# Performance work log

Measured on AMD Instinct MI355X. Metric: run time of the kernel, lower is better.

## Reference

```python
import jax, jax.numpy as jnp
import numpy as np
from jax import lax

BN_EPS = 1e-5
SP_NEAR = 2


def fps(xyz, m):
    # xyz: [b, n, c] -> indices [b, m]; deterministic start at index 0
    b, n, _ = xyz.shape
    def step(carry, _):
        dist, far = carry
        centroid = jnp.take_along_axis(xyz, far[:, None, None], axis=1)  # [b,1,c]
        d = jnp.sum((xyz - centroid) ** 2, axis=-1)                      # [b,n]
        dist = jnp.minimum(dist, d)
        return (dist, jnp.argmax(dist, axis=-1).astype(jnp.int32)), far
    init = (jnp.full((b, n), jnp.inf, xyz.dtype), jnp.zeros((b,), jnp.int32))
    _, idxs = lax.scan(step, init, None, length=m)
    return jnp.transpose(idxs)  # [b, m]


def knn(x, k):
    # x: [b, n, c] -> k nearest (incl. self) indices [b, n, k]
    sq = jnp.sum(x * x, axis=-1)
    d = sq[:, :, None] + sq[:, None, :] - 2.0 * jnp.einsum('bnc,bmc->bnm', x, x)
    return lax.top_k(-d, k)[1]


def gather_cf(x, idx):
    # channel-first index_points: x [b, c, n], idx [b, ...] -> [b, c, *idx.shape[1:]]
    b, c = x.shape[:2]
    flat = idx.reshape(b, -1)
    g = jnp.take_along_axis(x, flat[:, None, :], axis=2)
    return g.reshape((b, c) + idx.shape[1:])


def gather_cl(x, idx):
    # channel-last index_points: x [b, n, c], idx [b, ...] -> [b, *idx.shape[1:], c]
    b, c = x.shape[0], x.shape[-1]
    flat = idx.reshape(b, -1)
    g = jnp.take_along_axis(x, flat[:, :, None], axis=1)
    return g.reshape((b,) + idx.shape[1:] + (c,))


def bn_act(x, gamma, beta, nd):
    # inference-mode BatchNorm (running mean 0, var 1) + exact GELU; Dropout is identity in eval
    shp = (1, -1) + (1,) * nd
    scale = 1.0 / jnp.sqrt(1.0 + BN_EPS)
    return jax.nn.gelu(gamma.reshape(shp) * (x * scale) + beta.reshape(shp), approximate=False)


def setup_inputs() -> dict:
    key = jax.random.key(0)
    ks = jax.random.split(key, 8)
    BS, SP_IN, SP_OUT, DN_IN, DN_OUT = 128, 256, 256, 128, 128
    N_STK, N_STK_PNT, COOR = 32, 32, 32
    return {
        'sparse_fea': jax.random.normal(ks[0], (BS, SP_IN, N_STK), jnp.float32),
        'dense_fea': jax.random.normal(ks[1], (BS, DN_IN, N_STK, N_STK_PNT), jnp.float32),
        'stk_coor': jax.random.normal(ks[2], (BS, N_STK, COOR), jnp.float32),
        'n_stk_center': 16,
        'sp_w': jax.random.normal(ks[3], (SP_OUT, 2 * SP_IN), jnp.float32) * 0.02,
        'sp_b': jnp.zeros((SP_OUT,), jnp.float32),
        'sp_g': jnp.ones((SP_OUT,), jnp.float32),
        'sp_beta': jnp.zeros((SP_OUT,), jnp.float32),
        'dn_w': jax.random.normal(ks[4], (DN_OUT, 2 * DN_IN), jnp.float32) * 0.02,
        'dn_b': jnp.zeros((DN_OUT,), jnp.float32),
        'dn_g': jnp.ones((DN_OUT,), jnp.float32),
        'dn_beta': jnp.zeros((DN_OUT,), jnp.float32),
        'ds_w': jax.random.normal(ks[5], (DN_OUT, DN_IN, 1, 3), jnp.float32) * 0.05,
        'ds_b': jnp.zeros((DN_OUT,), jnp.float32),
        'ds_g': jnp.ones((DN_OUT,), jnp.float32),
        'ds_beta': jnp.zeros((DN_OUT,), jnp.float32),
    }


def reference(sparse_fea, dense_fea, stk_coor, n_stk_center,
              sp_w, sp_b, sp_g, sp_beta,
              dn_w, dn_b, dn_g, dn_beta,
              ds_w, ds_b, ds_g, ds_beta):
    bs, dn_in, n_stk, n_stk_pnt = dense_fea.shape
    fps_idx = fps(stk_coor, n_stk_center)            # [b, m]
    # --- sparse branch ---
    sc = gather_cf(sparse_fea, fps_idx)              # [b, c, m]
    knn_all = knn(stk_coor, SP_NEAR)                 # [b, n, k]
    knn_fps = gather_cl(knn_all, fps_idx)            # [b, m, k]
    sn = gather_cf(sparse_fea, knn_fps)              # [b, c, m, k]
    sa = sn - sc[:, :, :, None]
    sp_x = jnp.concatenate([sa, jnp.broadcast_to(sc[:, :, :, None], sa.shape)], axis=1)  # [b,2c,m,k]
    sp_x = jnp.einsum('bimk,oi->bomk', sp_x, sp_w) + sp_b[None, :, None, None]
    sp_x = bn_act(sp_x, sp_g, sp_beta, 2)
    sparse_out = jnp.max(sp_x, axis=3)               # [b, sp_out, m]
    # --- dense branch ---
    # 'b c s sp -> b s (sp c)'
    d_flat = jnp.transpose(dense_fea, (0, 2, 3, 1)).reshape(bs, n_stk, n_stk_pnt * dn_in)
    dc = gather_cl(d_flat, fps_idx)                  # [b, m, sp*c]
    dnb = gather_cl(d_flat, knn_fps)                 # [b, m, k, sp*c]
    da = dnb - dc[:, :, None, :]
    dcat = jnp.concatenate([da, jnp.broadcast_to(dc[:, :, None, :], da.shape)], axis=3)  # [b,m,k,2*sp*c]
    # 'b s n (sp c) -> b c s sp n' with sp=n_stk_pnt (exact torch reshape semantics)
    d5 = dcat.reshape(bs, fps_idx.shape[1], SP_NEAR, n_stk_pnt, 2 * dn_in)
    d5 = jnp.transpose(d5, (0, 4, 1, 3, 2))          # [b, 2c, m, sp, k]
    d5 = jnp.einsum('bimpn,oi->bompn', d5, dn_w) + dn_b[None, :, None, None, None]
    d5 = bn_act(d5, dn_g, dn_beta, 3)
    d4 = jnp.max(d5, axis=4)                         # [b, dn_out, m, sp]
    y = lax.conv_general_dilated(d4, ds_w, window_strides=(1, 2), padding=((0, 0), (1, 1)),
                                 dimension_numbers=('NCHW', 'OIHW', 'NCHW')) + ds_b[None, :, None, None]
    dense_out = bn_act(y, ds_g, ds_beta, 2)          # [b, dn_out, m, sp//2]
    coor_out = gather_cl(stk_coor, fps_idx)          # [b, m, coor]
    return sparse_out, dense_out, coor_out
```

## Files before the change

kernel.cpp:

```cpp
#include <hip/hip_runtime.h>


typedef unsigned short u16;
typedef unsigned int   u32;
typedef __attribute__((ext_vector_type(8))) short bf16x8;
typedef __attribute__((ext_vector_type(4))) float f32x4;

#define BN_SCALE 0.9999950000374997f

__device__ __forceinline__ float gelu_f(float x){
  return 0.5f*x*(1.0f + erff(x*0.70710678118654752f));
}
__device__ __forceinline__ u16 f2bf(float f){
  u32 x = __float_as_uint(f);
  x += 0x7fffu + ((x>>16)&1u);
  return (u16)(x>>16);
}
#define MFMA16(a,b,c) __builtin_amdgcn_mfma_f32_16x16x32_bf16(a,b,c,0,0,0)

__global__ __launch_bounds__(256) void k_prep(
    const float* __restrict__ dn_w, const float* __restrict__ ds_w, const float* __restrict__ sp_w,
    const float* __restrict__ coor,
    u16* __restrict__ wdb, u16* __restrict__ wcb, u16* __restrict__ wsb,
    int* __restrict__ fps_idx, int* __restrict__ nn_idx, float* __restrict__ coor_out)
{
  int blk = blockIdx.x, t = threadIdx.x;
  if (blk < 128){
    int w = blk*256 + t;
    int j=w&7, lane=(w>>3)&63, tile=w>>9;
    int kt=tile>>3, ot=tile&7;
    int o=ot*16+(lane&15), i=kt*32+((lane>>4)&3)*8+j;
    wdb[w] = f2bf(dn_w[o*256+i]);
  } else if (blk < 320){
    int w = (blk-128)*256 + t;
    int j=w&7, lane=(w>>3)&63, tile=w>>9;
    int kt=tile>>3, ot=tile&7;
    int o=ot*16+(lane&15), k=kt*32+((lane>>4)&3)*8+j;
    wcb[w] = f2bf(ds_w[o*384+k]);
  } else if (blk < 832){
    int w = (blk-320)*256 + t;
    int j=w&7, lane=(w>>3)&63, tile=w>>9;
    int kt=tile>>4, ot=tile&15;
    int o=ot*16+(lane&15), i=kt*32+((lane>>4)&3)*8+j;
    wsb[w] = f2bf(sp_w[o*512+i]);
  } else {
    int b = blk - 832;
    __shared__ float Xs[32*33];
    __shared__ float D[32*33];
    __shared__ int   s_sel[16];
    for (int i=t;i<1024;i+=256) Xs[(i>>5)*33 + (i&31)] = coor[b*1024+i];
    __syncthreads();
    #pragma unroll
    for (int k2=0;k2<4;k2++){
      int p=t+k2*256, i=p>>5, j=p&31;
      float d=0.f;
      #pragma unroll
      for (int c=0;c<32;c++){ float df=Xs[i*33+c]-Xs[j*33+c]; d+=df*df; }
      D[i*33+j]=d;
    }
    __syncthreads();
    if (t < 64){
      int j = t & 31;
      float dist = 3.0e38f;
      int far = 0;
      #pragma unroll
      for (int it=0; it<16; ++it){
        if (t==0) s_sel[it]=far;
        dist = fminf(dist, D[far*33+j]);
        float v=dist; int idx=j;
        #pragma unroll
        for (int off=16; off>=1; off>>=1){
          float v2=__shfl_xor(v,off,32); int i2=__shfl_xor(idx,off,32);
          if (v2>v || (v2==v && i2<idx)){ v=v2; idx=i2; }
        }
        far = idx;
      }
      if (t==0){
        #pragma unroll
        for (int it=0;it<16;++it) fps_idx[b*16+it]=s_sel[it];
      }
    }
    __syncthreads();
    {
      int wv=t>>6, j=t&31;
      #pragma unroll
      for (int q=0;q<4;q++){
        int it = wv*4+q, sel = s_sel[it];
        float d = D[sel*33+j];
        if (j==sel) d=3.0e38f;
        float v=d; int idx=j;
        #pragma unroll
        for (int off=16; off>=1; off>>=1){
          float v2=__shfl_xor(v,off,32); int i2=__shfl_xor(idx,off,32);
          if (v2<v || (v2==v && i2<idx)){ v=v2; idx=i2; }
        }
        if ((t&63)==0) nn_idx[b*16+it]=idx;
      }
    }
    for (int q=t;q<512;q+=256){
      int mm=q>>5, c=q&31;
      coor_out[b*512+q] = Xs[s_sel[mm]*33 + c];
    }
  }
}

__global__ __launch_bounds__(256) void k_main(
    const float* __restrict__ sfea, const u16* __restrict__ wsb,
    const float* __restrict__ sp_b, const float* __restrict__ sp_g, const float* __restrict__ sp_be,
    const float* __restrict__ dfea, const u16* __restrict__ wdb,
    const float* __restrict__ dn_b, const float* __restrict__ dn_g, const float* __restrict__ dn_be,
    const u16* __restrict__ wcb,
    const float* __restrict__ ds_b, const float* __restrict__ ds_g, const float* __restrict__ ds_be,
    const int* __restrict__ fps_idx, const int* __restrict__ nn_idx,
    float* __restrict__ out_sp, float* __restrict__ out_dn)
{
  __shared__ char smem[19456];
  __shared__ int SI[32];
  int blk=blockIdx.x;
  int t=threadIdx.x, lane=t&63, wv=t>>6, quad=lane>>4, col=lane&15;
  if (blk < 128){
    int b = blk;
    u16*   Xb = (u16*)smem;
    float* P  = (float*)(smem+16640);
    if (t<32){
      SI[t] = ((t<16) ? fps_idx[b*16+t] : nn_idx[b*16+(t-16)]) & 31;
    }
    { float A = sp_g[t]*BN_SCALE; P[t]=A; P[256+t]=fmaf(sp_b[t],A,sp_be[t]); }
    __syncthreads();
    {
      const float* row = sfea + b*8192 + t*32;
      #pragma unroll 1
      for (int m=0;m<16;m++){
        float vc=row[SI[m]], vn=row[SI[16+m]];
        Xb[m*520 + t]       = f2bf(vn-vc);
        Xb[m*520 + 256 + t] = f2bf(vc);
      }
    }
    __syncthreads();
    #pragma unroll 1
    for (int oh=0;oh<2;oh++){
      f32x4 accA[2]={}, accB[2]={};
      #pragma unroll 1
      for (int kt=0;kt<8;kt++){
        bf16x8 bf0 = *(const bf16x8*)&Xb[col*520 + kt*32 + quad*8];
        bf16x8 a0  = *(const bf16x8*)&wsb[((kt*16 + oh*8 + wv    )*64+lane)*8];
        bf16x8 a1  = *(const bf16x8*)&wsb[((kt*16 + oh*8 + wv + 4)*64+lane)*8];
        accA[0]=MFMA16(a0,bf0,accA[0]); accA[1]=MFMA16(a1,bf0,accA[1]);
      }
      #pragma unroll 1
      for (int kt=8;kt<16;kt++){
        bf16x8 bf0 = *(const bf16x8*)&Xb[col*520 + kt*32 + quad*8];
        bf16x8 a0  = *(const bf16x8*)&wsb[((kt*16 + oh*8 + wv    )*64+lane)*8];
        bf16x8 a1  = *(const bf16x8*)&wsb[((kt*16 + oh*8 + wv + 4)*64+lane)*8];
        accB[0]=MFMA16(a0,bf0,accB[0]); accB[1]=MFMA16(a1,bf0,accB[1]);
      }
      #pragma unroll
      for (int r=0;r<2;r++){
        #pragma unroll
        for (int reg=0;reg<4;reg++){
          int o = oh*128 + (wv+r*4)*16 + quad*4 + reg;
          float A=P[o], Bv=P[256+o];
          float k1 = accA[r][reg]+accB[r][reg];
          float k0 = accB[r][reg];
          float v = fmaxf(gelu_f(fmaf(k1,A,Bv)), gelu_f(fmaf(k0,A,Bv)));
          out_sp[(b*256+o)*16 + col] = v;
        }
      }
    }
  } else {
    int d=blk-128;
    int b = ((d>>7)<<3) | (d&7), m = (d>>3)&15;
    u16* Vb = (u16*)smem;
    u16* Bc = (u16*)smem;
    float* Pd = (float*)(smem+16896);
    int ci=fps_idx[b*16+m]&31, ni=nn_idx[b*16+m]&31;
    if (t < 128){
      float A  = dn_g[t]*BN_SCALE; float Bv = fmaf(dn_b[t], A, dn_be[t]);
      float Ac = ds_g[t]*BN_SCALE; float Cv = fmaf(ds_b[t], Ac, ds_be[t]);
      Pd[t]=A; Pd[128+t]=Bv; Pd[256+t]=Ac; Pd[384+t]=Cv;
      Pd[512+t]=gelu_f(Bv);
    }
    const float* Db = dfea + b*131072;
    #pragma unroll 1
    for (int it=0; it<2; it++){
      int w = t + it*256;
      int c = (w>>3)*2, x = (w&7)*4;
      const float* base = Db + c*1024 + x;
      float4 fcA = *(const float4*)(base + ci*32);
      float4 fnA = *(const float4*)(base + ni*32);
      float4 fcB = *(const float4*)(base + 1024 + ci*32);
      float4 fnB = *(const float4*)(base + 1024 + ni*32);
      #pragma unroll
      for (int e=0;e<4;e++){
        int xx=x+e, dp=xx&1, p=xx>>1;
        u32 dlo = f2bf(((const float*)&fnA)[e] - ((const float*)&fcA)[e]);
        u32 dhi = f2bf(((const float*)&fnB)[e] - ((const float*)&fcB)[e]);
        u32 clo = f2bf(((const float*)&fcA)[e]);
        u32 chi = f2bf(((const float*)&fcB)[e]);
        *(u32*)&Vb[p*264 + dp*128 + c]      = dlo | (dhi<<16);
        *(u32*)&Vb[(16+p)*264 + dp*128 + c] = clo | (chi<<16);
      }
    }
    __syncthreads();
    f32x4 acc[2][2]={};
    #pragma unroll 1
    for (int kt=0;kt<8;kt++){
      bf16x8 a0 = *(const bf16x8*)&wdb[((kt*8+wv  )*64+lane)*8];
      bf16x8 a1 = *(const bf16x8*)&wdb[((kt*8+wv+4)*64+lane)*8];
      bf16x8 b0 = *(const bf16x8*)&Vb[col*264      + kt*32 + quad*8];
      bf16x8 b1 = *(const bf16x8*)&Vb[(16+col)*264 + kt*32 + quad*8];
      acc[0][0]=MFMA16(a0,b0,acc[0][0]); acc[0][1]=MFMA16(a0,b1,acc[0][1]);
      acc[1][0]=MFMA16(a1,b0,acc[1][0]); acc[1][1]=MFMA16(a1,b1,acc[1][1]);
    }
    __syncthreads();
    if (t<128) Bc[t*3] = 0;
    #pragma unroll
    for (int r=0;r<2;r++){
      #pragma unroll
      for (int pt=0;pt<2;pt++){
        #pragma unroll
        for (int reg=0;reg<4;reg++){
          int o = (wv+r*4)*16 + quad*4 + reg;
          int p = pt*16 + col;
          float val = gelu_f(fmaf(acc[r][pt][reg], Pd[o], Pd[128+o]));
          if (pt==0) val = fmaxf(val, Pd[512+o]);
          u16 bv = f2bf(val);
          if (p&1){
            Bc[((p-1)>>1)*392 + o*3 + 2] = bv;
            if (p<31) Bc[((p+1)>>1)*392 + o*3 + 0] = bv;
          } else {
            Bc[(p>>1)*392 + o*3 + 1] = bv;
          }
        }
      }
    }
    __syncthreads();
    f32x4 cacc[2]={};
    #pragma unroll 1
    for (int kt=0;kt<12;kt++){
      bf16x8 cb0 = *(const bf16x8*)&Bc[col*392 + kt*32 + quad*8];
      bf16x8 a0  = *(const bf16x8*)&wcb[((kt*8+wv  )*64+lane)*8];
      bf16x8 a1  = *(const bf16x8*)&wcb[((kt*8+wv+4)*64+lane)*8];
      cacc[0]=MFMA16(a0,cb0,cacc[0]);
      cacc[1]=MFMA16(a1,cb0,cacc[1]);
    }
    #pragma unroll
    for (int r=0;r<2;r++){
      #pragma unroll
      for (int reg=0;reg<4;reg++){
        int o = (wv+r*4)*16 + quad*4 + reg;
        float val = gelu_f(fmaf(cacc[r][reg], Pd[256+o], Pd[384+o]));
        out_dn[(b*128+o)*256 + m*16 + col] = val;
      }
    }
  }
}

extern "C" void kernel_launch(void* const* d_in, const int* in_sizes, int n_in,
                              void* d_out, int out_size, void* d_ws, size_t ws_size,
                              hipStream_t stream) {
  const float* sparse_fea = (const float*)d_in[0];
  const float* dense_fea  = (const float*)d_in[1];
  const float* stk_coor   = (const float*)d_in[2];
  const float* sp_w  = (const float*)d_in[4];
  const float* sp_b  = (const float*)d_in[5];
  const float* sp_g  = (const float*)d_in[6];
  const float* sp_be = (const float*)d_in[7];
  const float* dn_w  = (const float*)d_in[8];
  const float* dn_b  = (const float*)d_in[9];
  const float* dn_g  = (const float*)d_in[10];
  const float* dn_be = (const float*)d_in[11];
  const float* ds_w  = (const float*)d_in[12];
  const float* ds_b  = (const float*)d_in[13];
  const float* ds_g  = (const float*)d_in[14];
  const float* ds_be = (const float*)d_in[15];

  float* out = (float*)d_out;
  int* fps_idx = (int*)d_ws;
  int* nn_idx  = fps_idx + 2048;
  u16* wdb = (u16*)((char*)d_ws + 16384);
  u16* wcb = (u16*)((char*)d_ws + 81920);
  u16* wsb = (u16*)((char*)d_ws + 180224);

  k_prep<<<960, 256, 0, stream>>>(dn_w, ds_w, sp_w, stk_coor,
                                  wdb, wcb, wsb, fps_idx, nn_idx, out + 4718592);
  k_main<<<2176, 256, 0, stream>>>(sparse_fea, wsb, sp_b, sp_g, sp_be,
                                   dense_fea, wdb, dn_b, dn_g, dn_be,
                                   wcb, ds_b, ds_g, ds_be,
                                   fps_idx, nn_idx, out, out + 524288);
}
```

Measured before the change: 159.3 us.

## Process two centers per dense block and software-pipeline gathers with MFMA stages

Each dense-branch block now handles two sampled centers instead of one, which halves the block count. The second center's global gathers are issued before the first GEMM, and its first GEMM is interleaved with the first center's downsample-conv GEMM. The goal is to hide global load latency and keep the MFMA units busy across stages. In exchange, shared memory nearly doubles and register pressure rises, which can lower occupancy, and the grid drops from 2176 to 1152 blocks.

```diff
diff --git a/kernel.cpp b/kernel.cpp
--- a/kernel.cpp
+++ b/kernel.cpp
@@ -17,6 +17,38 @@
   return (u16)(x>>16);
 }
 #define MFMA16(a,b,c) __builtin_amdgcn_mfma_f32_16x16x32_bf16(a,b,c,0,0,0)
+
+#define PACK8(VB, fcL, fnL, fcH, fnH, C, X) do{                                   \
+  _Pragma("unroll") for (int e=0;e<4;e++){                                        \
+    int xx=(X)+e, dp=xx&1, p=xx>>1;                                               \
+    u32 dv = (u32)f2bf(((const float*)&(fnL))[e]-((const float*)&(fcL))[e])       \
+           | ((u32)f2bf(((const float*)&(fnH))[e]-((const float*)&(fcH))[e])<<16);\
+    u32 cv = (u32)f2bf(((const float*)&(fcL))[e])                                 \
+           | ((u32)f2bf(((const float*)&(fcH))[e])<<16);                          \
+    *(u32*)&(VB)[p*264 + dp*128 + (C)]      = dv;                                 \
+    *(u32*)&(VB)[(16+p)*264 + dp*128 + (C)] = cv;                                 \
+  } }while(0)
+
+#define EPI1(ACC, BC) do{                                                         \
+  _Pragma("unroll") for (int r=0;r<2;r++){                                        \
+    _Pragma("unroll") for (int pt=0;pt<2;pt++){                                   \
+      _Pragma("unroll") for (int reg=0;reg<4;reg++){                              \
+        int o=(wv+r*4)*16+quad*4+reg; int p=pt*16+col;                            \
+        float val=gelu_f(fmaf((ACC)[r][pt][reg], Pd[o], Pd[128+o]));              \
+        if (pt==0) val=fmaxf(val, Pd[512+o]);                                     \
+        u16 bv=f2bf(val);                                                         \
+        if (p&1){ (BC)[((p-1)>>1)*392+o*3+2]=bv;                                  \
+                  if(p<31)(BC)[((p+1)>>1)*392+o*3+0]=bv; }                        \
+        else    { (BC)[(p>>1)*392+o*3+1]=bv; }                                    \
+      } } } }while(0)
+
+#define EPI2(CACC, MM) do{                                                        \
+  _Pragma("unroll") for (int r=0;r<2;r++){                                        \
+    _Pragma("unroll") for (int reg=0;reg<4;reg++){                                \
+      int o=(wv+r*4)*16+quad*4+reg;                                               \
+      float val=gelu_f(fmaf((CACC)[r][reg], Pd[256+o], Pd[384+o]));               \
+      out_dn[(b*128+o)*256 + (MM)*16 + col]=val;                                  \
+    } } }while(0)
 
 __global__ __launch_bounds__(256) void k_prep(
     const float* __restrict__ dn_w, const float* __restrict__ ds_w, const float* __restrict__ sp_w,
@@ -114,7 +146,7 @@
     const int* __restrict__ fps_idx, const int* __restrict__ nn_idx,
     float* __restrict__ out_sp, float* __restrict__ out_dn)
 {
-  __shared__ char smem[19456];
+  __shared__ char smem[36352];
   __shared__ int SI[32];
   int blk=blockIdx.x;
   int t=threadIdx.x, lane=t&63, wv=t>>6, quad=lane>>4, col=lane&15;
@@ -169,11 +201,14 @@
     }
   } else {
     int d=blk-128;
-    int b = ((d>>7)<<3) | (d&7), m = (d>>3)&15;
-    u16* Vb = (u16*)smem;
-    u16* Bc = (u16*)smem;
-    float* Pd = (float*)(smem+16896);
-    int ci=fps_idx[b*16+m]&31, ni=nn_idx[b*16+m]&31;
+    int b = ((d>>6)<<3) | (d&7), m0 = ((d>>3)&7)*2;
+    u16* Vb0 = (u16*)smem;
+    u16* Vb1 = (u16*)(smem+16896);
+    u16* Bc0 = Vb0;
+    u16* Bc1 = Vb1;
+    float* Pd = (float*)(smem+33792);
+    int ciA=fps_idx[b*16+m0]&31,   niA=nn_idx[b*16+m0]&31;
+    int ciB=fps_idx[b*16+m0+1]&31, niB=nn_idx[b*16+m0+1]&31;
     if (t < 128){
       float A  = dn_g[t]*BN_SCALE; float Bv = fmaf(dn_b[t], A, dn_be[t]);
       float Ac = ds_g[t]*BN_SCALE; float Cv = fmaf(ds_b[t], Ac, ds_be[t]);
@@ -181,78 +216,72 @@
       Pd[512+t]=gelu_f(Bv);
     }
     const float* Db = dfea + b*131072;
-    #pragma unroll 1
-    for (int it=0; it<2; it++){
-      int w = t + it*256;
-      int c = (w>>3)*2, x = (w&7)*4;
-      const float* base = Db + c*1024 + x;
-      float4 fcA = *(const float4*)(base + ci*32);
-      float4 fnA = *(const float4*)(base + ni*32);
-      float4 fcB = *(const float4*)(base + 1024 + ci*32);
-      float4 fnB = *(const float4*)(base + 1024 + ni*32);
-      #pragma unroll
-      for (int e=0;e<4;e++){
-        int xx=x+e, dp=xx&1, p=xx>>1;
-        u32 dlo = f2bf(((const float*)&fnA)[e] - ((const float*)&fcA)[e]);
-        u32 dhi = f2bf(((const float*)&fnB)[e] - ((const float*)&fcB)[e]);
-        u32 clo = f2bf(((const float*)&fcA)[e]);
-        u32 chi = f2bf(((const float*)&fcB)[e]);
-        *(u32*)&Vb[p*264 + dp*128 + c]      = dlo | (dhi<<16);
-        *(u32*)&Vb[(16+p)*264 + dp*128 + c] = clo | (chi<<16);
-      }
-    }
-    __syncthreads();
-    f32x4 acc[2][2]={};
+    int c0=(t>>3)*2,        x0=(t&7)*4;
+    int w1=t+256; int c1=(w1>>3)*2, x1=(w1&7)*4;
+    const float* base0 = Db + c0*1024 + x0;
+    const float* base1 = Db + c1*1024 + x1;
+    {
+      float4 fc=*(const float4*)(base0+ciA*32), fn=*(const float4*)(base0+niA*32);
+      float4 gc=*(const float4*)(base0+1024+ciA*32), gn=*(const float4*)(base0+1024+niA*32);
+      PACK8(Vb0, fc, fn, gc, gn, c0, x0);
+      fc=*(const float4*)(base1+ciA*32); fn=*(const float4*)(base1+niA*32);
+      gc=*(const float4*)(base1+1024+ciA*32); gn=*(const float4*)(base1+1024+niA*32);
+      PACK8(Vb0, fc, fn, gc, gn, c1, x1);
+    }
+    float4 gB0=*(const float4*)(base0+ciB*32),      gB1=*(const float4*)(base0+niB*32);
+    float4 gB2=*(const float4*)(base0+1024+ciB*32), gB3=*(const float4*)(base0+1024+niB*32);
+    float4 gB4=*(const float4*)(base1+ciB*32),      gB5=*(const float4*)(base1+niB*32);
+    float4 gB6=*(const float4*)(base1+1024+ciB*32), gB7=*(const float4*)(base1+1024+niB*32);
+    __syncthreads();
+    f32x4 accA[2][2]={};
     #pragma unroll 1
     for (int kt=0;kt<8;kt++){
       bf16x8 a0 = *(const bf16x8*)&wdb[((kt*8+wv  )*64+lane)*8];
       bf16x8 a1 = *(const bf16x8*)&wdb[((kt*8+wv+4)*64+lane)*8];
-      bf16x8 b0 = *(const bf16x8*)&Vb[col*264      + kt*32 + quad*8];
-      bf16x8 b1 = *(const bf16x8*)&Vb[(16+col)*264 + kt*32 + quad*8];
-      acc[0][0]=MFMA16(a0,b0,acc[0][0]); acc[0][1]=MFMA16(a0,b1,acc[0][1]);
-      acc[1][0]=MFMA16(a1,b0,acc[1][0]); acc[1][1]=MFMA16(a1,b1,acc[1][1]);
-    }
-    __syncthreads();
-    if (t<128) Bc[t*3] = 0;
-    #pragma unroll
-    for (int r=0;r<2;r++){
-      #pragma unroll
-      for (int pt=0;pt<2;pt++){
-        #pragma unroll
-        for (int reg=0;reg<4;reg++){
-          int o = (wv+r*4)*16 + quad*4 + reg;
-          int p = pt*16 + col;
-          float val = gelu_f(fmaf(acc[r][pt][reg], Pd[o], Pd[128+o]));
-          if (pt==0) val = fmaxf(val, Pd[512+o]);
-          u16 bv = f2bf(val);
-          if (p&1){
-            Bc[((p-1)>>1)*392 + o*3 + 2] = bv;
-            if (p<31) Bc[((p+1)>>1)*392 + o*3 + 0] = bv;
-          } else {
-            Bc[(p>>1)*392 + o*3 + 1] = bv;
-          }
-        }
-      }
-    }
+      bf16x8 b0 = *(const bf16x8*)&Vb0[col*264      + kt*32 + quad*8];
+      bf16x8 b1 = *(const bf16x8*)&Vb0[(16+col)*264 + kt*32 + quad*8];
+      accA[0][0]=MFMA16(a0,b0,accA[0][0]); accA[0][1]=MFMA16(a0,b1,accA[0][1]);
+      accA[1][0]=MFMA16(a1,b0,accA[1][0]); accA[1][1]=MFMA16(a1,b1,accA[1][1]);
+    }
+    __syncthreads();
+    PACK8(Vb1, gB0, gB1, gB2, gB3, c0, x0);
+    PACK8(Vb1, gB4, gB5, gB6, gB7, c1, x1);
+    if (t<128) Bc0[t*3] = 0;
+    EPI1(accA, Bc0);
     __syncthreads();
     f32x4 cacc[2]={};
+    f32x4 accB[2][2]={};
     #pragma unroll 1
     for (int kt=0;kt<12;kt++){
-      bf16x8 cb0 = *(const bf16x8*)&Bc[col*392 + kt*32 + quad*8];
-      bf16x8 a0  = *(const bf16x8*)&wcb[((kt*8+wv  )*64+lane)*8];
-      bf16x8 a1  = *(const bf16x8*)&wcb[((kt*8+wv+4)*64+lane)*8];
-      cacc[0]=MFMA16(a0,cb0,cacc[0]);
-      cacc[1]=MFMA16(a1,cb0,cacc[1]);
-    }
-    #pragma unroll
-    for (int r=0;r<2;r++){
-      #pragma unroll
-      for (int reg=0;reg<4;reg++){
-        int o = (wv+r*4)*16 + quad*4 + reg;
-        float val = gelu_f(fmaf(cacc[r][reg], Pd[256+o], Pd[384+o]));
-        out_dn[(b*128+o)*256 + m*16 + col] = val;
-      }
-    }
+      bf16x8 cb0 = *(const bf16x8*)&Bc0[col*392 + kt*32 + quad*8];
+      bf16x8 ca0 = *(const bf16x8*)&wcb[((kt*8+wv  )*64+lane)*8];
+      bf16x8 ca1 = *(const bf16x8*)&wcb[((kt*8+wv+4)*64+lane)*8];
+      cacc[0]=MFMA16(ca0,cb0,cacc[0]);
+      cacc[1]=MFMA16(ca1,cb0,cacc[1]);
+      if (kt<8){
+        bf16x8 a0 = *(const bf16x8*)&wdb[((kt*8+wv  )*64+lane)*8];
+        bf16x8 a1 = *(const bf16x8*)&wdb[((kt*8+wv+4)*64+lane)*8];
+        bf16x8 b0 = *(const bf16x8*)&Vb1[col*264      + kt*32 + quad*8];
+        bf16x8 b1 = *(const bf16x8*)&Vb1[(16+col)*264 + kt*32 + quad*8];
+        accB[0][0]=MFMA16(a0,b0,accB[0][0]); accB[0][1]=MFMA16(a0,b1,accB[0][1]);
+        accB[1][0]=MFMA16(a1,b0,accB[1][0]); accB[1][1]=MFMA16(a1,b1,accB[1][1]);
+      }
+    }
+    __syncthreads();
+    if (t<128) Bc1[t*3] = 0;
+    EPI1(accB, Bc1);
+    EPI2(cacc, m0);
+    __syncthreads();
+    f32x4 cacc2[2]={};
+    #pragma unroll 1
+    for (int kt=0;kt<12;kt++){
+      bf16x8 cb0 = *(const bf16x8*)&Bc1[col*392 + kt*32 + quad*8];
+      bf16x8 ca0 = *(const bf16x8*)&wcb[((kt*8+wv  )*64+lane)*8];
+      bf16x8 ca1 = *(const bf16x8*)&wcb[((kt*8+wv+4)*64+lane)*8];
+      cacc2[0]=MFMA16(ca0,cb0,cacc2[0]);
+      cacc2[1]=MFMA16(ca1,cb0,cacc2[1]);
+    }
+    EPI2(cacc2, m0+1);
   }
 }
 
@@ -284,7 +313,7 @@
 
   k_prep<<<960, 256, 0, stream>>>(dn_w, ds_w, sp_w, stk_coor,
                                   wdb, wcb, wsb, fps_idx, nn_idx, out + 4718592);
-  k_main<<<2176, 256, 0, stream>>>(sparse_fea, wsb, sp_b, sp_g, sp_be,
+  k_main<<<1152, 256, 0, stream>>>(sparse_fea, wsb, sp_b, sp_g, sp_be,
                                    dense_fea, wdb, dn_b, dn_g, dn_be,
                                    wcb, ds_b, ds_g, ds_be,
                                    fps_idx, nn_idx, out, out + 524288);
```

Measured after the change: 171.5 us. +7.7%, slower.
